# Optimization experiments

Measured on AMD Instinct MI355X. Metric: run time of the kernel, lower is better.

The kernel has to match this reference:

```python
import jax, jax.numpy as jnp
import numpy as np

NUM_HEADS = 8
EPS = 1e-5


def conv3x3(x, w):
    # x: (b,c,f,w), w: (out_c,in_c,3,3), padding=1, stride=1, no bias
    return jax.lax.conv_general_dilated(
        x, w, window_strides=(1, 1), padding=((1, 1), (1, 1)),
        dimension_numbers=('NCHW', 'OIHW', 'NCHW'))


def mc_layernorm(x, g, b):
    # MultichannelLayerNorm: layernorm over the feature axis (dim 2),
    # per-(channel, feature) affine.
    m = jnp.mean(x, axis=2, keepdims=True)
    v = jnp.var(x, axis=2, keepdims=True)
    xn = (x - m) * jax.lax.rsqrt(v + EPS)
    return xn * g[None, :, :, None] + b[None, :, :, None]


def mc_linear(x, wp, wd=None):
    # per-channel feature linear: y[b,c,g,w] = sum_f wp[c,g,f] x[b,c,f,w]
    y = jnp.einsum('bcfw,cgf->bcgw', x, wp)
    if wd is not None:  # depthwise=True adds 1x1 cross-channel mix
        y = jnp.einsum('bcfw,oc->bofw', y, wd)
    return y


def _split_heads(t):
    # (b,c,f,w) -> (b,c,w,H,dh); matches transpose(2,3).reshape(b,c,w,H,-1)
    b, c, f, w = t.shape
    return jnp.transpose(t, (0, 1, 3, 2)).reshape(b, c, w, NUM_HEADS, f // NUM_HEADS)


def _forward(x, conv_q, conv_k, conv_v, wq, wk, wv, wo_pw, wo_dw,
             g1, b1, g2, b2, w1_pw, w1_dw, w2_pw):
    b, c, f, w = x.shape
    # --- attention (MultichannelMultiheadAttention, prev_qk=None) ---
    n1 = mc_layernorm(x, g1, b1)
    q = _split_heads(mc_linear(conv3x3(n1, conv_q), wq))  # (b,c,w,H,dh)
    k = _split_heads(mc_linear(conv3x3(n1, conv_k), wk))
    v = _split_heads(mc_linear(conv3x3(n1, conv_v), wv))
    # qk: (b,c,H,w,w); scaled by sqrt(features) (torch uses sqrt(h)=height)
    qk = jnp.einsum('bcqhd,bckhd->bchqk', q, k) / jnp.sqrt(jnp.float32(f))
    a = jnp.einsum('bchqk,bckhd->bcqhd', jax.nn.softmax(qk, axis=-1), v)
    a = jnp.transpose(a.reshape(b, c, w, f), (0, 1, 3, 2))  # (b,c,f,w)
    z = mc_linear(a, wo_pw, wo_dw)  # o_proj, depthwise=True
    h = x + z  # dropout is identity in eval
    # --- FFN with SquaredReLU ---
    n2 = mc_layernorm(h, g2, b2)
    u = mc_linear(n2, w1_pw, w1_dw)          # (b,c,4f,w)
    u = jnp.square(jax.nn.relu(u))           # SquaredReLU
    z = mc_linear(u, w2_pw)                  # (b,c,f,w)
    h = h + z
    return h, qk


def setup_inputs() -> dict:
    key = jax.random.key(0)
    ks = jax.random.split(key, 12)
    b, c, f, w = 2, 16, 256, 512
    e = 4 * f
    s_conv = 1.0 / np.sqrt(c * 9)
    s_f = 1.0 / np.sqrt(f)
    s_e = 1.0 / np.sqrt(e)
    s_c = 1.0 / np.sqrt(c)
    return {
        'x': jax.random.normal(ks[0], (b, c, f, w), jnp.float32),
        'conv_q': jax.random.normal(ks[1], (c, c, 3, 3), jnp.float32) * s_conv,
        'conv_k': jax.random.normal(ks[2], (c, c, 3, 3), jnp.float32) * s_conv,
        'conv_v': jax.random.normal(ks[3], (c, c, 3, 3), jnp.float32) * s_conv,
        'wq': jax.random.normal(ks[4], (c, f, f), jnp.float32) * s_f,
        'wk': jax.random.normal(ks[5], (c, f, f), jnp.float32) * s_f,
        'wv': jax.random.normal(ks[6], (c, f, f), jnp.float32) * s_f,
        'wo_pw': jax.random.normal(ks[7], (c, f, f), jnp.float32) * s_f,
        'wo_dw': jax.random.normal(ks[8], (c, c), jnp.float32) * s_c,
        'g1': jnp.ones((c, f), jnp.float32),
        'b1': jnp.zeros((c, f), jnp.float32),
        'g2': jnp.ones((c, f), jnp.float32),
        'b2': jnp.zeros((c, f), jnp.float32),
        'w1_pw': jax.random.normal(ks[9], (c, e, f), jnp.float32) * s_f,
        'w1_dw': jax.random.normal(ks[10], (c, c), jnp.float32) * s_c,
        'w2_pw': jax.random.normal(ks[11], (c, f, e), jnp.float32) * s_e,
    }


def reference(x, conv_q, conv_k, conv_v, wq, wk, wv, wo_pw, wo_dw,
              g1, b1, g2, b2, w1_pw, w1_dw, w2_pw):
    return _forward(x, conv_q, conv_k, conv_v, wq, wk, wv, wo_pw, wo_dw,
                    g1, b1, g2, b2, w1_pw, w1_dw, w2_pw)
```

## Files before the change

kernel.cpp:

```cpp
#include <hip/hip_runtime.h>

#define BB 2
#define CC 16
#define BC 32
#define FF 256
#define WW 512
#define HH 8
#define DH 32

using bf16x8 = __attribute__((ext_vector_type(8))) __bf16;
using f32x4  = __attribute__((ext_vector_type(4))) float;
using us8    = __attribute__((ext_vector_type(8))) unsigned short;
using us4    = __attribute__((ext_vector_type(4))) unsigned short;

#define AS1 __attribute__((address_space(1)))
#define AS3 __attribute__((address_space(3)))

__device__ __forceinline__ float bf2f(unsigned short u) {
    union { unsigned int i; float f; } x; x.i = ((unsigned int)u) << 16; return x.f;
}
__device__ __forceinline__ unsigned short f2bf(float f) {
    union { float f; unsigned int i; } x; x.f = f;
    unsigned int r = x.i + 0x7fffu + ((x.i >> 16) & 1u);
    return (unsigned short)(r >> 16);
}
__device__ __forceinline__ f32x4 mfma16(bf16x8 a, bf16x8 b, f32x4 c) {
    return __builtin_amdgcn_mfma_f32_16x16x32_bf16(a, b, c, 0, 0, 0);
}
__device__ __forceinline__ void gload16(const void* g, void* l) {
    __builtin_amdgcn_global_load_lds((AS1 void*)g, (AS3 void*)l, 16, 0, 0);
}

__global__ __launch_bounds__(256) void prep_ln(
    const float* __restrict__ x, const float* __restrict__ g1,
    const float* __restrict__ b1, unsigned short* __restrict__ n1,
    const float* __restrict__ wq, const float* __restrict__ wk,
    const float* __restrict__ wv, const float* __restrict__ wo,
    const float* __restrict__ w1, const float* __restrict__ w2,
    const float* __restrict__ cwq, const float* __restrict__ cwk,
    const float* __restrict__ cwv,
    unsigned short* __restrict__ Wqkv, unsigned short* __restrict__ Wo16,
    unsigned short* __restrict__ W116, unsigned short* __restrict__ W216,
    unsigned short* __restrict__ Aw) {
    __shared__ float red[2][4][64];
    __shared__ float mr[2][64];
    int bid = blockIdx.x;
    if (bid < 256) {
        int bc = bid & 31, c = bc & 15;
        int part = threadIdx.x >> 6, wl = threadIdx.x & 63;
        int w = (bid >> 5) * 64 + wl;
        const float* xp = x + ((size_t)bc * FF + part * 64) * WW + w;
        float s = 0.f, s2 = 0.f;
#pragma unroll 4
        for (int i = 0; i < 64; ++i) { float t = xp[(size_t)i * WW]; s += t; s2 += t * t; }
        red[0][part][wl] = s; red[1][part][wl] = s2;
        __syncthreads();
        if (part == 0) {
            float S  = red[0][0][wl] + red[0][1][wl] + red[0][2][wl] + red[0][3][wl];
            float S2 = red[1][0][wl] + red[1][1][wl] + red[1][2][wl] + red[1][3][wl];
            float m = S * (1.f / FF);
            float v = S2 * (1.f / FF) - m * m;
            mr[0][wl] = m; mr[1][wl] = rsqrtf(v + 1e-5f);
        }
        __syncthreads();
        float m = mr[0][wl], r = mr[1][wl];
        const float* gp = g1 + c * FF + part * 64;
        const float* bp = b1 + c * FF + part * 64;
        unsigned short* op = n1 + ((size_t)bc * FF + part * 64) * WW + w;
#pragma unroll 4
        for (int i = 0; i < 64; ++i)
            op[(size_t)i * WW] = f2bf((xp[(size_t)i * WW] - m) * r * gp[i] + bp[i]);
    } else if (bid < 256 + 6144) {
        int i = (bid - 256) * 256 + threadIdx.x;
        const float* s; unsigned short* d; int off;
        if (i < 131072)       { s = wq; d = Wqkv;            off = i; }
        else if (i < 262144)  { s = wk; d = Wqkv + 1048576;  off = i - 131072; }
        else if (i < 393216)  { s = wv; d = Wqkv + 2097152;  off = i - 262144; }
        else if (i < 524288)  { s = wo; d = Wo16;            off = i - 393216; }
        else if (i < 1048576) { s = w1; d = W116;            off = i - 524288; }
        else                  { s = w2; d = W216;            off = i - 1048576; }
        const float4* sp = (const float4*)s + (size_t)off * 2;
        float4 a = sp[0], b = sp[1];
        us8 p;
        p[0] = f2bf(a.x); p[1] = f2bf(a.y); p[2] = f2bf(a.z); p[3] = f2bf(a.w);
        p[4] = f2bf(b.x); p[5] = f2bf(b.y); p[6] = f2bf(b.z); p[7] = f2bf(b.w);
        *((us8*)d + off) = p;
    } else {
        int idx = (bid - 256 - 6144) * 256 + threadIdx.x;
        if (idx < 7680) {
            int tensor = idx / 2560;
            int r = idx - tensor * 2560;
            int tp = r >> 9, co = (r >> 5) & 15, k = r & 31;
            int tap = tp * 2 + (k >> 4), ci = k & 15;
            float v = 0.f;
            if (tap < 9) {
                const float* w = tensor == 0 ? cwq : (tensor == 1 ? cwk : cwv);
                v = w[(co * 16 + ci) * 9 + tap];
            }
            Aw[idx] = f2bf(v);
        }
    }
}

__global__ __launch_bounds__(256) void ln2t_kernel(
    const float* __restrict__ x, const float* __restrict__ g,
    const float* __restrict__ bta, unsigned short* __restrict__ out) {
    __shared__ float red[2][4][64];
    __shared__ float mr[2][64];
    int bc = blockIdx.x, c = bc & 15;
    int part = threadIdx.x >> 6, wl = threadIdx.x & 63;
    int w = blockIdx.y * 64 + wl;
    const float* xp = x + ((size_t)bc * FF + part * 64) * WW + w;
    float s = 0.f, s2 = 0.f;
#pragma unroll 4
    for (int i = 0; i < 64; ++i) { float t = xp[(size_t)i * WW]; s += t; s2 += t * t; }
    red[0][part][wl] = s; red[1][part][wl] = s2;
    __syncthreads();
    if (part == 0) {
        float S  = red[0][0][wl] + red[0][1][wl] + red[0][2][wl] + red[0][3][wl];
        float S2 = red[1][0][wl] + red[1][1][wl] + red[1][2][wl] + red[1][3][wl];
        float m = S * (1.f / FF);
        float v = S2 * (1.f / FF) - m * m;
        mr[0][wl] = m; mr[1][wl] = rsqrtf(v + 1e-5f);
    }
    __syncthreads();
    float m = mr[0][wl], r = mr[1][wl];
    const float* gp = g + c * FF + part * 64;
    const float* bp = bta + c * FF + part * 64;
    unsigned short* op = out + ((size_t)bc * WW + w) * FF + part * 64;
    for (int i8 = 0; i8 < 8; ++i8) {
        us8 pk;
#pragma unroll
        for (int e = 0; e < 8; ++e) {
            int i = i8 * 8 + e;
            pk[e] = f2bf((xp[(size_t)i * WW] - m) * r * gp[i] + bp[i]);
        }
        *(us8*)(op + i8 * 8) = pk;
    }
}

__global__ __launch_bounds__(256) void conv3_mfma(
    const unsigned short* __restrict__ n1, const unsigned short* __restrict__ Aw,
    unsigned short* __restrict__ oq, unsigned short* __restrict__ ok,
    unsigned short* __restrict__ ov) {
    __shared__ __align__(16) unsigned short Xl[6][68][16];
    const int b = blockIdx.z;
    const int f0 = blockIdx.y * 4;
    const int w0 = blockIdx.x * 64;
    const int tx = threadIdx.x;
    const int lane = tx & 63, wid = tx >> 6;
    const int lr = lane & 15, lg = lane >> 4;
    {
        uint4 z{0, 0, 0, 0};
        for (int i = tx; i < 816; i += 256) ((uint4*)Xl)[i] = z;
    }
    __syncthreads();
    for (int task = tx; task < 960; task += 256) {
        int c = task % 10;
        int fr = (task / 10) % 6;
        int ci = task / 60;
        int fy = f0 - 1 + fr;
        int wx = w0 - 8 + c * 8;
        if (fy >= 0 && fy < FF && wx >= 0 && wx <= WW - 8) {
            us8 v = *(const us8*)(n1 + ((size_t)(b * CC + ci) * FF + fy) * WW + wx);
#pragma unroll
            for (int e = 0; e < 8; ++e) {
                int wl = c * 8 + e - 7;
                if (wl >= 0 && wl < 66) Xl[fr][wl][ci] = v[e];
            }
        }
    }
    __syncthreads();
    bf16x8 A[3][5];
#pragma unroll
    for (int t3 = 0; t3 < 3; ++t3)
#pragma unroll
        for (int t = 0; t < 5; ++t)
            A[t3][t] = *(const bf16x8*)(Aw + ((t3 * 5 + t) * 16 + lr) * 32 + lg * 8);
    const bool h = (lane & 32) != 0;
    int doff[5];
    doff[0] = (h ? (-68 * 32) : ((-68 - 1) * 32));
    doff[1] = (h ? (-1 * 32) : ((-68 + 1) * 32));
    doff[2] = (h ? (1 * 32) : 0);
    doff[3] = (h ? (68 * 32) : ((68 - 1) * 32));
    doff[4] = ((68 + 1) * 32);
    const int fl = wid + 1;
    const int fglob = f0 + wid;
    char* xbase = (char*)Xl + (fl * 68 + 1) * 32 + ((lg & 1) ? 16 : 0);
#pragma unroll
    for (int pt = 0; pt < 4; ++pt) {
        char* bb = xbase + (pt * 16 + lr) * 32;
        bf16x8 Bf[5];
#pragma unroll
        for (int t = 0; t < 5; ++t) Bf[t] = *(const bf16x8*)(bb + doff[t]);
        f32x4 aq = {0.f, 0.f, 0.f, 0.f}, ak = {0.f, 0.f, 0.f, 0.f}, av = {0.f, 0.f, 0.f, 0.f};
#pragma unroll
        for (int t = 0; t < 5; ++t) {
            aq = mfma16(A[0][t], Bf[t], aq);
            ak = mfma16(A[1][t], Bf[t], ak);
            av = mfma16(A[2][t], Bf[t], av);
        }
        int w = w0 + pt * 16 + lr;
#pragma unroll
        for (int r = 0; r < 4; ++r) {
            int co = lg * 4 + r;
            size_t o = ((size_t)(b * CC + co) * FF + fglob) * WW + w;
            oq[o] = f2bf(aq[r]);
            ok[o] = f2bf(ak[r]);
            ov[o] = f2bf(av[r]);
        }
    }
}

template <int K, int BSRC, int MODE, int NT>
__global__ __launch_bounds__(256, 3) void mgemm3(
    const unsigned short* __restrict__ Wb, const unsigned short* __restrict__ T,
    unsigned short* __restrict__ ob, float* __restrict__ of) {
    constexpr int M = 256;
    __shared__ __align__(16) unsigned short Al[64 * 64];
    __shared__ __align__(16) unsigned short Bl[128 * 64];
    const int id = blockIdx.x;
    const int grp = ((id >> 5) << 3) | (id & 7);
    const int g = (id >> 3) & 3;
    const int t = (NT > 1) ? (grp >> 7) : 0;
    const int rem = grp & 127;
    const int bc = rem >> 2, z = rem & 3;
    const int c = bc & 15;
    const int G0 = g * 64, W0 = z * 128;
    const int tx = threadIdx.x;
    const int lane = tx & 63, wid = tx >> 6;
    const int lr = lane & 15, lg = lane >> 4;
    const int wr = wid >> 1, wc = wid & 1;
    const unsigned short* Ab = Wb + (size_t)t * 1048576 + ((size_t)c * M + G0) * K;
    const unsigned short* Tt = T + (size_t)t * 4194304;
    f32x4 acc[2][4];
#pragma unroll
    for (int i = 0; i < 2; ++i)
#pragma unroll
        for (int j = 0; j < 4; ++j) acc[i][j] = (f32x4){0.f, 0.f, 0.f, 0.f};

    const int arow0 = tx >> 3;
    const int aseg0 = (tx & 7) ^ (arow0 & 7);
    const int bsegx = (tx & 7) ^ (arow0 & 7) ^ ((arow0 >> 3) & 7);

    for (int f0 = 0; f0 < K; f0 += 64) {
#pragma unroll
        for (int rep = 0; rep < 2; ++rep) {
            int row = arow0 + rep * 32;
            int seg = (tx & 7) ^ (row & 7);
            gload16(Ab + (size_t)row * K + f0 + seg * 8,
                    (char*)Al + wid * 1024 + rep * 4096);
        }
        if (BSRC == 0) {
            const unsigned short* Tb = Tt + ((size_t)bc * WW + W0) * K;
#pragma unroll
            for (int rep = 0; rep < 4; ++rep) {
                int row = arow0 + rep * 32;
                int seg = (tx & 7) ^ (row & 7) ^ ((row >> 3) & 7);
                gload16(Tb + (size_t)row * K + f0 + seg * 8,
                        (char*)Bl + wid * 1024 + rep * 4096);
            }
        } else {
            const unsigned short* Tb = Tt + (size_t)bc * K * WW;
            const int wseg = tx & 15, fgrp = tx >> 4;
            us8 tv[4];
#pragma unroll
            for (int i = 0; i < 4; ++i)
                tv[i] = *(const us8*)(Tb + (size_t)(f0 + fgrp * 4 + i) * WW + W0 + wseg * 8);
#pragma unroll
            for (int j = 0; j < 8; ++j) {
                int w = wseg * 8 + j;
                us4 p; p.x = tv[0][j]; p.y = tv[1][j]; p.z = tv[2][j]; p.w = tv[3][j];
                *(us4*)((char*)Bl + w * 128 +
                        ((((fgrp >> 1) ^ (w & 7) ^ ((w >> 3) & 7)) << 4)) + (fgrp & 1) * 8) = p;
            }
        }
        __syncthreads();
#pragma unroll
        for (int kc = 0; kc < 2; ++kc) {
            bf16x8 af[2], bf[4];
#pragma unroll
            for (int i = 0; i < 2; ++i) {
                int gr = wr * 32 + i * 16 + lr;
                af[i] = *(const bf16x8*)((char*)Al + gr * 128 +
                        (((kc * 4 + lg) ^ (gr & 7)) << 4));
            }
#pragma unroll
            for (int j = 0; j < 4; ++j) {
                int wrw = wc * 64 + j * 16 + lr;
                bf[j] = *(const bf16x8*)((char*)Bl + wrw * 128 +
                        (((kc * 4 + lg) ^ (wrw & 7) ^ ((wrw >> 3) & 7)) << 4));
            }
#pragma unroll
            for (int i = 0; i < 2; ++i)
#pragma unroll
                for (int j = 0; j < 4; ++j)
                    acc[i][j] = mfma16(af[i], bf[j], acc[i][j]);
        }
        __syncthreads();
    }
#pragma unroll
    for (int i = 0; i < 2; ++i)
#pragma unroll
        for (int j = 0; j < 4; ++j) {
            int g2 = G0 + wr * 32 + i * 16 + lg * 4;
            int w = W0 + wc * 64 + j * 16 + lr;
#pragma unroll
            for (int r = 0; r < 4; ++r) {
                size_t o = (size_t)t * 4194304 + ((size_t)bc * M + g2 + r) * WW + w;
                if (MODE == 0) ob[o] = f2bf(acc[i][j][r]);
                else of[o] += acc[i][j][r];
            }
        }
}

template <int K, int M, int MODE>
__global__ __launch_bounds__(256, 2) void mgemm2(
    const unsigned short* __restrict__ Wb, const unsigned short* __restrict__ T,
    unsigned short* __restrict__ ob, float* __restrict__ of) {
    __shared__ __align__(16) unsigned short Al[128 * 64];
    __shared__ __align__(16) unsigned short Bl[128 * 64];
    const int id = blockIdx.x;
    const int grp = ((id >> 6) << 3) | (id & 7);
    const int g = (id >> 3) & 7;
    const int bc = grp >> 2, z = grp & 3;
    const int c = bc & 15;
    const int G0 = g * 128, W0 = z * 128;
    const int tx = threadIdx.x;
    const int lane = tx & 63, wid = tx >> 6;
    const int lr = lane & 15, lg = lane >> 4;
    const int wr = wid >> 1, wc = wid & 1;
    const unsigned short* Ab = Wb + ((size_t)c * M + G0) * K;
    f32x4 acc[4][4];
#pragma unroll
    for (int i = 0; i < 4; ++i)
#pragma unroll
        for (int j = 0; j < 4; ++j) acc[i][j] = (f32x4){0.f, 0.f, 0.f, 0.f};

    const int arow0 = tx >> 3;

    for (int f0 = 0; f0 < K; f0 += 64) {
#pragma unroll
        for (int rep = 0; rep < 4; ++rep) {
            int row = arow0 + rep * 32;
            int seg = (tx & 7) ^ (row & 7);
            gload16(Ab + (size_t)row * K + f0 + seg * 8,
                    (char*)Al + wid * 1024 + rep * 4096);
        }
        {
            const unsigned short* Tb = T + ((size_t)bc * WW + W0) * K;
#pragma unroll
            for (int rep = 0; rep < 4; ++rep) {
                int row = arow0 + rep * 32;
                int seg = (tx & 7) ^ (row & 7) ^ ((row >> 3) & 7);
                gload16(Tb + (size_t)row * K + f0 + seg * 8,
                        (char*)Bl + wid * 1024 + rep * 4096);
            }
        }
        __syncthreads();
#pragma unroll
        for (int kc = 0; kc < 2; ++kc) {
            bf16x8 af[4], bf[4];
#pragma unroll
            for (int i = 0; i < 4; ++i) {
                int gr = wr * 64 + i * 16 + lr;
                af[i] = *(const bf16x8*)((char*)Al + gr * 128 +
                        (((kc * 4 + lg) ^ (gr & 7)) << 4));
                int wrw = wc * 64 + i * 16 + lr;
                bf[i] = *(const bf16x8*)((char*)Bl + wrw * 128 +
                        (((kc * 4 + lg) ^ (wrw & 7) ^ ((wrw >> 3) & 7)) << 4));
            }
#pragma unroll
            for (int i = 0; i < 4; ++i)
#pragma unroll
                for (int j = 0; j < 4; ++j)
                    acc[i][j] = mfma16(af[i], bf[j], acc[i][j]);
        }
        __syncthreads();
    }
#pragma unroll
    for (int i = 0; i < 4; ++i)
#pragma unroll
        for (int j = 0; j < 4; ++j) {
            int gg = G0 + wr * 64 + i * 16 + lg * 4;
            int w = W0 + wc * 64 + j * 16 + lr;
            if (MODE == 2) {
                us4 pk;
                pk.x = f2bf(acc[i][j][0]); pk.y = f2bf(acc[i][j][1]);
                pk.z = f2bf(acc[i][j][2]); pk.w = f2bf(acc[i][j][3]);
                *(us4*)(ob + ((size_t)bc * WW + w) * M + gg) = pk;
            } else {
#pragma unroll
                for (int r = 0; r < 4; ++r) {
                    size_t o = ((size_t)bc * M + gg + r) * WW + w;
                    if (MODE == 0) ob[o] = f2bf(acc[i][j][r]);
                    else of[o] += acc[i][j][r];
                }
            }
        }
}

__global__ __launch_bounds__(256, 2) void attn_fused(
    const unsigned short* __restrict__ qb, const unsigned short* __restrict__ kb,
    const unsigned short* __restrict__ vb, float* __restrict__ qko,
    unsigned short* __restrict__ abT) {
    __shared__ unsigned short Kl[512 * 32];
    __shared__ unsigned short Vl[32 * 512];
    __shared__ unsigned short Ql[64 * 32];
    const int bch = blockIdx.x, qt = blockIdx.y;
    const int bc = bch >> 3, h = bch & 7;
    const int tx = threadIdx.x;
    const int lane = tx & 63, wid = tx >> 6;
    const int lr = lane & 15, lg = lane >> 4;

    const unsigned short* kbase = kb + ((size_t)bc * FF + h * DH) * WW;
    const unsigned short* vbase = vb + ((size_t)bc * FF + h * DH) * WW;
    const unsigned short* qbase = qb + ((size_t)bc * FF + h * DH) * WW + qt * 64;

    {
        int d0 = ((tx >> 3) & 7) * 4;
#pragma unroll
        for (int rep = 0; rep < 2; ++rep) {
            int kw0 = (tx & 7) * 8 + ((tx >> 6) & 3) * 64 + rep * 256;
            us8 v0 = *(const us8*)(kbase + (size_t)(d0 + 0) * WW + kw0);
            us8 v1 = *(const us8*)(kbase + (size_t)(d0 + 1) * WW + kw0);
            us8 v2 = *(const us8*)(kbase + (size_t)(d0 + 2) * WW + kw0);
            us8 v3 = *(const us8*)(kbase + (size_t)(d0 + 3) * WW + kw0);
#pragma unroll
            for (int j = 0; j < 8; ++j) {
                int kw = kw0 + j;
                us4 p; p.x = v0[j]; p.y = v1[j]; p.z = v2[j]; p.w = v3[j];
                *(us4*)((char*)Kl + kw * 64 + ((d0 * 2) ^ ((kw & 3) << 4))) = p;
            }
        }
    }
    {
        int d = tx >> 3;
        int sw = (d & 7) << 4;
#pragma unroll
        for (int rep = 0; rep < 8; ++rep) {
            int kw0 = (tx & 7) * 8 + rep * 64;
            us8 tv = *(const us8*)(vbase + (size_t)d * WW + kw0);
            *(us8*)((char*)Vl + d * 1024 + ((kw0 * 2) ^ sw)) = tv;
        }
    }
    if (tx < 64) {
        int d0 = ((tx >> 3) & 7) * 4;
        int q0 = (tx & 7) * 8;
        us8 v0 = *(const us8*)(qbase + (size_t)(d0 + 0) * WW + q0);
        us8 v1 = *(const us8*)(qbase + (size_t)(d0 + 1) * WW + q0);
        us8 v2 = *(const us8*)(qbase + (size_t)(d0 + 2) * WW + q0);
        us8 v3 = *(const us8*)(qbase + (size_t)(d0 + 3) * WW + q0);
#pragma unroll
        for (int j = 0; j < 8; ++j) {
            us4 p; p.x = v0[j]; p.y = v1[j]; p.z = v2[j]; p.w = v3[j];
            *(us4*)(&Ql[(q0 + j) * 32 + d0]) = p;
        }
    }
    __syncthreads();

    const int q0w = wid * 16;
    bf16x8 qf = *(const bf16x8*)((char*)Ql + (q0w + lr) * 64 + lg * 16);
    f32x4 s[32];
#pragma unroll
    for (int i = 0; i < 32; ++i) s[i] = (f32x4){0.f, 0.f, 0.f, 0.f};
#pragma unroll
    for (int kwt = 0; kwt < 32; ++kwt) {
        int krow = kwt * 16 + lr;
        bf16x8 kf = *(const bf16x8*)((char*)Kl + krow * 64 + ((lg * 16) ^ ((krow & 3) << 4)));
        s[kwt] = mfma16(kf, qf, s[kwt]);
    }
    float mx = -3.0e38f;
    float* qrow = qko + ((size_t)bch * WW + qt * 64 + q0w + lr) * WW;
#pragma unroll
    for (int kwt = 0; kwt < 32; ++kwt) {
        s[kwt] *= 0.0625f;
        float4 st;
        st.x = s[kwt][0]; st.y = s[kwt][1]; st.z = s[kwt][2]; st.w = s[kwt][3];
        *(float4*)(qrow + kwt * 16 + lg * 4) = st;
        mx = fmaxf(mx, fmaxf(fmaxf(st.x, st.y), fmaxf(st.z, st.w)));
    }
    mx = fmaxf(mx, __shfl_xor(mx, 16));
    mx = fmaxf(mx, __shfl_xor(mx, 32));
    float sum = 0.f;
#pragma unroll
    for (int kwt = 0; kwt < 32; ++kwt) {
#pragma unroll
        for (int r = 0; r < 4; ++r) {
            float p = __expf(s[kwt][r] - mx);
            s[kwt][r] = p;
            sum += p;
        }
    }
    sum += __shfl_xor(sum, 16);
    sum += __shfl_xor(sum, 32);
    float inv = 1.0f / sum;

    f32x4 av[2];
    av[0] = (f32x4){0.f, 0.f, 0.f, 0.f};
    av[1] = (f32x4){0.f, 0.f, 0.f, 0.f};
#pragma unroll
    for (int t = 0; t < 16; ++t) {
        unsigned pa0 = f2bf(s[2 * t][0]) | ((unsigned)f2bf(s[2 * t][1]) << 16);
        unsigned pa1 = f2bf(s[2 * t][2]) | ((unsigned)f2bf(s[2 * t][3]) << 16);
        unsigned pb0 = f2bf(s[2 * t + 1][0]) | ((unsigned)f2bf(s[2 * t + 1][1]) << 16);
        unsigned pb1 = f2bf(s[2 * t + 1][2]) | ((unsigned)f2bf(s[2 * t + 1][3]) << 16);
        unsigned s16_0 = (lg == 1) ? pa0 : pb0, s16_1 = (lg == 1) ? pa1 : pb1;
        unsigned s32_0 = (lg == 3) ? pa0 : pb0, s32_1 = (lg == 3) ? pa1 : pb1;
        unsigned s48_0 = (lg == 2) ? pa0 : pb0, s48_1 = (lg == 2) ? pa1 : pb1;
        unsigned r16_0 = (unsigned)__shfl_xor((int)s16_0, 16);
        unsigned r16_1 = (unsigned)__shfl_xor((int)s16_1, 16);
        unsigned r32_0 = (unsigned)__shfl_xor((int)s32_0, 32);
        unsigned r32_1 = (unsigned)__shfl_xor((int)s32_1, 32);
        unsigned r48_0 = (unsigned)__shfl_xor((int)s48_0, 48);
        unsigned r48_1 = (unsigned)__shfl_xor((int)s48_1, 48);
        uint4 wv;
        if (lg == 0)      { wv.x = pa0;   wv.y = pa1;   wv.z = r16_0; wv.w = r16_1; }
        else if (lg == 1) { wv.x = r48_0; wv.y = r48_1; wv.z = r32_0; wv.w = r32_1; }
        else if (lg == 2) { wv.x = r32_0; wv.y = r32_1; wv.z = r48_0; wv.w = r48_1; }
        else              { wv.x = r16_0; wv.y = r16_1; wv.z = pb0;  wv.w = pb1; }
        bf16x8 pf = *reinterpret_cast<bf16x8*>(&wv);
#pragma unroll
        for (int di = 0; di < 2; ++di) {
            int vr = di * 16 + lr;
            bf16x8 vf = *(const bf16x8*)((char*)Vl + vr * 1024 + ((t * 64 + lg * 16) ^ ((vr & 7) << 4)));
            av[di] = mfma16(vf, pf, av[di]);
        }
    }
    unsigned short* arow = abT + ((size_t)bc * WW + qt * 64 + q0w + lr) * FF + h * DH;
#pragma unroll
    for (int di = 0; di < 2; ++di) {
        us4 pk;
        pk.x = f2bf(av[di][0] * inv); pk.y = f2bf(av[di][1] * inv);
        pk.z = f2bf(av[di][2] * inv); pk.w = f2bf(av[di][3] * inv);
        *(us4*)(arow + di * 16 + lg * 4) = pk;
    }
}

template <int NPC, int MODE>
__global__ __launch_bounds__(256) void dwmix(
    const unsigned short* __restrict__ in, const float* __restrict__ wdw,
    const float* __restrict__ x, float* __restrict__ fo, unsigned short* __restrict__ bo) {
    __shared__ unsigned short L[16][1024];
    int b = blockIdx.y;
    size_t base = (size_t)blockIdx.x * 1024;
    int tx = threadIdx.x;
#pragma unroll
    for (int r = 0; r < 8; ++r) {
        int idx = tx + r * 256;
        int ci = idx >> 7;
        int seg = idx & 127;
        *(us8*)&L[ci][seg * 8] = *(const us8*)(in + ((size_t)(b * 16 + ci)) * NPC + base + seg * 8);
    }
    __syncthreads();
#pragma unroll
    for (int pos = 0; pos < 4; ++pos) {
        int fw = tx + pos * 256;
        float vin[16];
#pragma unroll
        for (int ci = 0; ci < 16; ++ci) vin[ci] = bf2f(L[ci][fw]);
#pragma unroll
        for (int o = 0; o < 16; ++o) {
            float s = 0.f;
#pragma unroll
            for (int ci = 0; ci < 16; ++ci) s += wdw[o * 16 + ci] * vin[ci];
            size_t oi = ((size_t)(b * 16 + o)) * NPC + base + fw;
            if (MODE == 0) fo[oi] = x[oi] + s;
            else { s = fmaxf(s, 0.f); bo[oi] = f2bf(s * s); }
        }
    }
}

extern "C" void kernel_launch(void* const* d_in, const int* in_sizes, int n_in,
                              void* d_out, int out_size, void* d_ws, size_t ws_size,
                              hipStream_t stream) {
    const float* x      = (const float*)d_in[0];
    const float* conv_q = (const float*)d_in[1];
    const float* conv_k = (const float*)d_in[2];
    const float* conv_v = (const float*)d_in[3];
    const float* wq     = (const float*)d_in[4];
    const float* wk     = (const float*)d_in[5];
    const float* wv     = (const float*)d_in[6];
    const float* wo_pw  = (const float*)d_in[7];
    const float* wo_dw  = (const float*)d_in[8];
    const float* g1     = (const float*)d_in[9];
    const float* b1     = (const float*)d_in[10];
    const float* g2     = (const float*)d_in[11];
    const float* b2     = (const float*)d_in[12];
    const float* w1_pw  = (const float*)d_in[13];
    const float* w1_dw  = (const float*)d_in[14];
    const float* w2_pw  = (const float*)d_in[15];

    float* hout  = (float*)d_out;
    float* qkout = (float*)d_out + 4194304;

    char* ws = (char*)d_ws;
    const size_t MB1 = (size_t)1 << 20;
    unsigned short* n1   = (unsigned short*)(ws + 0 * MB1);
    unsigned short* cq   = (unsigned short*)(ws + 8 * MB1);
    unsigned short* qb   = (unsigned short*)(ws + 32 * MB1);
    unsigned short* kb   = (unsigned short*)(ws + 40 * MB1);
    unsigned short* vb   = (unsigned short*)(ws + 48 * MB1);
    unsigned short* abT  = (unsigned short*)(ws + 56 * MB1);
    unsigned short* pwb  = (unsigned short*)(ws + 64 * MB1);
    unsigned short* n2t  = (unsigned short*)(ws + 72 * MB1);
    unsigned short* u1t  = (unsigned short*)(ws + 80 * MB1);
    unsigned short* u2t  = (unsigned short*)(ws + 112 * MB1);
    unsigned short* Wqkv = (unsigned short*)(ws + 144 * MB1);
    unsigned short* Wo16 = (unsigned short*)(ws + 150 * MB1);
    unsigned short* W116 = (unsigned short*)(ws + 152 * MB1);
    unsigned short* W216 = (unsigned short*)(ws + 160 * MB1);
    unsigned short* Awb  = (unsigned short*)(ws + 168 * MB1);

    prep_ln<<<dim3(6430), 256, 0, stream>>>(x, g1, b1, n1,
                                            wq, wk, wv, wo_pw, w1_pw, w2_pw,
                                            conv_q, conv_k, conv_v,
                                            Wqkv, Wo16, W116, W216, Awb);
    conv3_mfma<<<dim3(8, 64, BB), 256, 0, stream>>>(n1, Awb, cq, cq + 4194304, cq + 8388608);
    mgemm3<256, 1, 0, 3><<<dim3(1536), 256, 0, stream>>>(Wqkv, cq, qb, nullptr);
    attn_fused<<<dim3(BC * HH, 8), 256, 0, stream>>>(qb, kb, vb, qkout, abT);
    mgemm3<256, 0, 0, 1><<<dim3(512), 256, 0, stream>>>(Wo16, abT, pwb, nullptr);
    dwmix<131072, 0><<<dim3(128, BB), 256, 0, stream>>>(pwb, wo_dw, x, hout, nullptr);
    ln2t_kernel<<<dim3(BC, 8), 256, 0, stream>>>(hout, g2, b2, n2t);
    mgemm2<256, 1024, 2><<<dim3(1024), 256, 0, stream>>>(W116, n2t, u1t, nullptr);
    dwmix<524288, 1><<<dim3(512, BB), 256, 0, stream>>>(u1t, w1_dw, nullptr, nullptr, u2t);
    mgemm3<1024, 0, 1, 1><<<dim3(512), 256, 0, stream>>>(W216, u2t, nullptr, hout);
}
```

Measured before the change: 281.3 us.

## Vectorize conv input staging, stage mgemm2 transposed output via LDS, raise mgemm3 occupancy

The conv3 staging loop now has each thread load four input channels and write them into LDS as packed 4-element stores, replacing many scalar LDS writes. mgemm2 in MODE 2 writes the transposed bf16 output through a swizzled LDS buffer so global stores become full 16-byte row-contiguous writes instead of scattered 8-byte ones. mgemm3's launch bound minimum blocks per CU goes from 3 to 4, which may raise occupancy at the risk of register spills. Two unused variables are also removed.

```diff
diff --git a/kernel.cpp b/kernel.cpp
--- a/kernel.cpp
+++ b/kernel.cpp
@@ -155,18 +155,34 @@
         for (int i = tx; i < 816; i += 256) ((uint4*)Xl)[i] = z;
     }
     __syncthreads();
-    for (int task = tx; task < 960; task += 256) {
-        int c = task % 10;
-        int fr = (task / 10) % 6;
-        int ci = task / 60;
+    if (tx < 240) {
+        int c = tx % 10;
+        int fr = (tx / 10) % 6;
+        int ci0 = (tx / 60) * 4;
         int fy = f0 - 1 + fr;
         int wx = w0 - 8 + c * 8;
         if (fy >= 0 && fy < FF && wx >= 0 && wx <= WW - 8) {
-            us8 v = *(const us8*)(n1 + ((size_t)(b * CC + ci) * FF + fy) * WW + wx);
-#pragma unroll
-            for (int e = 0; e < 8; ++e) {
-                int wl = c * 8 + e - 7;
-                if (wl >= 0 && wl < 66) Xl[fr][wl][ci] = v[e];
+            const unsigned short* base = n1 + ((size_t)(b * CC + ci0) * FF + fy) * WW + wx;
+            us8 v0 = *(const us8*)(base);
+            us8 v1 = *(const us8*)(base + (size_t)FF * WW);
+            us8 v2 = *(const us8*)(base + (size_t)2 * FF * WW);
+            us8 v3 = *(const us8*)(base + (size_t)3 * FF * WW);
+            if (c >= 1 && c <= 8) {
+#pragma unroll
+                for (int e = 0; e < 8; ++e) {
+                    int wl = c * 8 + e - 7;
+                    us4 p; p.x = v0[e]; p.y = v1[e]; p.z = v2[e]; p.w = v3[e];
+                    *(us4*)(&Xl[fr][wl][ci0]) = p;
+                }
+            } else {
+#pragma unroll
+                for (int e = 0; e < 8; ++e) {
+                    int wl = c * 8 + e - 7;
+                    if (wl >= 0 && wl < 66) {
+                        us4 p; p.x = v0[e]; p.y = v1[e]; p.z = v2[e]; p.w = v3[e];
+                        *(us4*)(&Xl[fr][wl][ci0]) = p;
+                    }
+                }
             }
         }
     }
@@ -213,7 +229,7 @@
 }
 
 template <int K, int BSRC, int MODE, int NT>
-__global__ __launch_bounds__(256, 3) void mgemm3(
+__global__ __launch_bounds__(256, 4) void mgemm3(
     const unsigned short* __restrict__ Wb, const unsigned short* __restrict__ T,
     unsigned short* __restrict__ ob, float* __restrict__ of) {
     constexpr int M = 256;
@@ -240,8 +256,6 @@
         for (int j = 0; j < 4; ++j) acc[i][j] = (f32x4){0.f, 0.f, 0.f, 0.f};
 
     const int arow0 = tx >> 3;
-    const int aseg0 = (tx & 7) ^ (arow0 & 7);
-    const int bsegx = (tx & 7) ^ (arow0 & 7) ^ ((arow0 >> 3) & 7);
 
     for (int f0 = 0; f0 < K; f0 += 64) {
 #pragma unroll
@@ -318,8 +332,9 @@
 __global__ __launch_bounds__(256, 2) void mgemm2(
     const unsigned short* __restrict__ Wb, const unsigned short* __restrict__ T,
     unsigned short* __restrict__ ob, float* __restrict__ of) {
-    __shared__ __align__(16) unsigned short Al[128 * 64];
-    __shared__ __align__(16) unsigned short Bl[128 * 64];
+    __shared__ __align__(16) unsigned short SH[2][128 * 64];
+    unsigned short* Al = SH[0];
+    unsigned short* Bl = SH[1];
     const int id = blockIdx.x;
     const int grp = ((id >> 6) << 3) | (id & 7);
     const int g = (id >> 3) & 7;
@@ -378,18 +393,35 @@
         }
         __syncthreads();
     }
-#pragma unroll
-    for (int i = 0; i < 4; ++i)
-#pragma unroll
-        for (int j = 0; j < 4; ++j) {
-            int gg = G0 + wr * 64 + i * 16 + lg * 4;
-            int w = W0 + wc * 64 + j * 16 + lr;
-            if (MODE == 2) {
+    if (MODE == 2) {
+        char* S = (char*)SH;
+#pragma unroll
+        for (int i = 0; i < 4; ++i)
+#pragma unroll
+            for (int j = 0; j < 4; ++j) {
+                int wl = wc * 64 + j * 16 + lr;
+                int gl = wr * 64 + i * 16 + lg * 4;
                 us4 pk;
                 pk.x = f2bf(acc[i][j][0]); pk.y = f2bf(acc[i][j][1]);
                 pk.z = f2bf(acc[i][j][2]); pk.w = f2bf(acc[i][j][3]);
-                *(us4*)(ob + ((size_t)bc * WW + w) * M + gg) = pk;
-            } else {
+                *(us4*)(S + wl * 256 + ((gl * 2) ^ ((wl & 7) << 4))) = pk;
+            }
+        __syncthreads();
+        unsigned short* og = ob + ((size_t)bc * WW + W0) * M + G0;
+#pragma unroll
+        for (int rep = 0; rep < 8; ++rep) {
+            int slot = tx + rep * 256;
+            int row = slot >> 4, col = slot & 15;
+            us8 v = *(const us8*)(S + row * 256 + ((col * 16) ^ ((row & 7) << 4)));
+            *(us8*)(og + (size_t)row * M + col * 8) = v;
+        }
+    } else {
+#pragma unroll
+        for (int i = 0; i < 4; ++i)
+#pragma unroll
+            for (int j = 0; j < 4; ++j) {
+                int gg = G0 + wr * 64 + i * 16 + lg * 4;
+                int w = W0 + wc * 64 + j * 16 + lr;
 #pragma unroll
                 for (int r = 0; r < 4; ++r) {
                     size_t o = ((size_t)bc * M + gg + r) * WW + w;
@@ -397,7 +429,7 @@
                     else of[o] += acc[i][j][r];
                 }
             }
-        }
+    }
 }
 
 __global__ __launch_bounds__(256, 2) void attn_fused(
```

Result: faster. 269.2 us (-4.3%).
